# Optimization experiments

Measured on AMD Instinct MI355X. Metric: run time of the kernel, lower is better.

The kernel has to match this reference:

```python
import jax, jax.numpy as jnp
import numpy as np

SEQ_LEN = 12
E, H, BOTTLE = 64, 128, 1024
G, P = 64, 24
B = G * P
EPS = 1e-12  # F.normalize eps


def setup_inputs() -> dict:
    key = jax.random.key(0)
    ks = jax.random.split(key, 24)
    r = lambda k, s: (jax.random.normal(k, s, dtype=jnp.float32) * 0.1)
    starts = np.arange(G, dtype=np.int64) * P
    seq_start_end = jnp.asarray(np.stack([starts, starts + P], axis=1))
    return {
        'last_pos': jax.random.normal(ks[0], (B, 2), dtype=jnp.float32),
        'last_pos_rel': jax.random.normal(ks[1], (B, 2), dtype=jnp.float32),
        'h0': jax.random.normal(ks[2], (1, B, H), dtype=jnp.float32),
        'c0': jax.random.normal(ks[3], (1, B, H), dtype=jnp.float32),
        'seq_start_end': seq_start_end,
        # decoder spatial embedding Linear(2, E)
        'W_emb': r(ks[4], (E, 2)), 'b_emb': r(ks[5], (E,)),
        # LSTM(E -> H), gates ordered i,f,g,o as in torch
        'W_ih': r(ks[6], (4 * H, E)), 'W_hh': r(ks[7], (4 * H, H)),
        'b_ih': r(ks[8], (4 * H,)), 'b_hh': r(ks[9], (4 * H,)),
        # hidden2pos Linear(H, 2)
        'W_pos': r(ks[10], (2, H)), 'b_pos': r(ks[11], (2,)),
        # pool_net spatial embedding Linear(2, E)
        'Wp_emb': r(ks[12], (E, 2)), 'bp_emb': r(ks[13], (E,)),
        # pool_net mlp_pre_pool: (E+H)->512->1024, ReLU
        'Wp1': r(ks[14], (512, E + H)), 'bp1': r(ks[15], (512,)),
        'Wp2': r(ks[16], (BOTTLE, 512)), 'bp2': r(ks[17], (BOTTLE,)),
        # decoder mlp: (H+BOTTLE)->1024->H, ReLU
        'Wm1': r(ks[18], (1024, H + BOTTLE)), 'bm1': r(ks[19], (1024,)),
        'Wm2': r(ks[20], (H, 1024)), 'bm2': r(ks[21], (H,)),
    }


def reference(last_pos, last_pos_rel, h0, c0, seq_start_end,
              W_emb, b_emb, W_ih, W_hh, b_ih, b_hh, W_pos, b_pos,
              Wp_emb, bp_emb, Wp1, bp1, Wp2, bp2, Wm1, bm1, Wm2, bm2):
    batch = last_pos.shape[0]
    n_grp = seq_start_end.shape[0]
    n_ped = batch // n_grp  # equal contiguous groups -> static reshape
    h_dim = h0.shape[-1]

    def pool_net(h, pos):
        # h: [B,H], pos: [B,2]; groups are contiguous slices of size n_ped
        pos_g = pos.reshape(n_grp, n_ped, 2)
        hid_g = h.reshape(n_grp, n_ped, h_dim)
        # rel[g,i,j] = pos[g,j] - pos[g,i]  (torch repeat semantics)
        rel = pos_g[:, None, :, :] - pos_g[:, :, None, :]  # [G,P,P,2]
        nrm = jnp.linalg.norm(rel, axis=-1, keepdims=True)
        rel = rel / jnp.maximum(nrm, EPS)
        emb = rel @ Wp_emb.T + bp_emb                       # [G,P,P,E]
        hid_b = jnp.broadcast_to(hid_g[:, None, :, :], (n_grp, n_ped, n_ped, h_dim))
        x = jnp.concatenate([emb, hid_b], axis=-1)          # [G,P,P,E+H]
        x = jax.nn.relu(x @ Wp1.T + bp1)
        x = jax.nn.relu(x @ Wp2.T + bp2)                    # [G,P,P,1024]
        return jnp.max(x, axis=2).reshape(batch, -1)        # max over j

    def lstm_step(x, h, c):
        gates = x @ W_ih.T + b_ih + h @ W_hh.T + b_hh
        i, f, g, o = jnp.split(gates, 4, axis=-1)
        c = jax.nn.sigmoid(f) * c + jax.nn.sigmoid(i) * jnp.tanh(g)
        h = jax.nn.sigmoid(o) * jnp.tanh(c)
        return h, c

    def step(carry, _):
        h, c, lp, dec_in = carry
        h, c = lstm_step(dec_in, h, c)
        rel_pos = h @ W_pos.T + b_pos          # [B,2]
        curr_pos = rel_pos + lp
        pool_h = pool_net(h, curr_pos)         # [B,1024]
        dh = jnp.concatenate([h, pool_h], axis=1)
        dh = jax.nn.relu(dh @ Wm1.T + bm1)
        h = jax.nn.relu(dh @ Wm2.T + bm2)      # refreshed hidden state
        dec_in = rel_pos @ W_emb.T + b_emb
        return (h, c, curr_pos, dec_in), rel_pos

    dec_in0 = last_pos_rel @ W_emb.T + b_emb
    (h, c, lp, di), rels = jax.lax.scan(
        step, (h0[0], c0[0], last_pos, dec_in0), None, length=SEQ_LEN)
    return rels, h[None]  # ([seq_len,B,2], [1,B,H])
```

## Files before the change

### kernel.cpp

```cpp
#include <hip/hip_runtime.h>
#include <hip/hip_bf16.h>

typedef __attribute__((ext_vector_type(4))) float f32x4;
typedef __attribute__((ext_vector_type(8))) _Float16 f16x8;

static __device__ __forceinline__ unsigned short h2u(_Float16 h) {
  union { _Float16 h; unsigned short u; } v; v.h = h; return v.u;
}


__global__ void cvt_split(const float* __restrict__ src, _Float16* __restrict__ dst, int n) {
  int i = blockIdx.x * 256 + threadIdx.x;
  if (i < n) {
    float x = src[i];
    _Float16 h = (_Float16)x;
    dst[i] = h;
    dst[(size_t)n + i] = (_Float16)(x - (float)h);
  }
}

__global__ void build_wg(const float* __restrict__ W_ih, const float* __restrict__ W_hh,
                         _Float16* __restrict__ Wg) {
  int i = blockIdx.x * 256 + threadIdx.x;
  if (i < 512 * 192) {
    int r = i / 192, k = i % 192;
    float v = (k < 64) ? W_ih[r * 64 + k] : W_hh[r * 128 + (k - 64)];
    _Float16 h = (_Float16)v;
    Wg[i] = h;
    Wg[512 * 192 + i] = (_Float16)(v - (float)h);
  }
}

__global__ void build_wp1b(const float* __restrict__ Wp1, _Float16* __restrict__ W) {
  int i = blockIdx.x * 256 + threadIdx.x;
  if (i < 512 * 128) {
    int r = i >> 7, k = i & 127;
    float v = Wp1[r * 192 + 64 + k];
    _Float16 h = (_Float16)v;
    W[i] = h;
    W[512 * 128 + i] = (_Float16)(v - (float)h);
  }
}

__global__ void build_w2f(const float* __restrict__ Wp2, _Float16* __restrict__ W2f) {
  int idx = blockIdx.x * 256 + threadIdx.x;
  if (idx >= 65536) return;
  int l = idx & 63;
  int c = (idx >> 6) & 15;
  int T = idx >> 10;
  int n = T * 16 + (l & 15);
  int kbase = c * 32 + (l >> 4) * 8;
  size_t dst = ((size_t)((T * 16 + c) * 2) * 64 + l) * 8;
  for (int e = 0; e < 8; e++) {
    float v = Wp2[(size_t)n * 512 + kbase + e];
    _Float16 h = (_Float16)v;
    W2f[dst + e] = h;
    W2f[dst + 512 + e] = (_Float16)(v - (float)h);
  }
}

__global__ void build_misc(const float* __restrict__ Wp1, const float* __restrict__ Wp_emb,
                           const float* __restrict__ bp_emb, const float* __restrict__ bp1,
                           const float* __restrict__ b_ih, const float* __restrict__ b_hh,
                           float* __restrict__ Uc, float* __restrict__ c1,
                           float* __restrict__ bias_g) {
  int r = blockIdx.x * 256 + threadIdx.x;
  if (r < 512) {
    float u0 = 0.f, u1 = 0.f, cc = 0.f;
    for (int e = 0; e < 64; e++) {
      float w = Wp1[r * 192 + e];
      u0 += w * Wp_emb[e * 2 + 0];
      u1 += w * Wp_emb[e * 2 + 1];
      cc += w * bp_emb[e];
    }
    Uc[r * 2 + 0] = u0;
    Uc[r * 2 + 1] = u1;
    c1[r] = bp1[r] + cc;
    bias_g[r] = b_ih[r] + b_hh[r];
  }
}

__global__ void init_state(const float* __restrict__ lp, const float* __restrict__ lpr,
                           const float* __restrict__ h0, const float* __restrict__ c0,
                           const float* __restrict__ W_emb, const float* __restrict__ b_emb,
                           _Float16* __restrict__ A_lstm, size_t PL_AL,
                           float* __restrict__ c_state, float* __restrict__ curr_pos) {
  int row = blockIdx.x;
  int t = threadIdx.x;
  float v;
  if (t < 64) {
    v = lpr[row * 2] * W_emb[t * 2] + lpr[row * 2 + 1] * W_emb[t * 2 + 1] + b_emb[t];
  } else {
    int u = t - 64;
    v = h0[(size_t)row * 128 + u];
    c_state[(size_t)row * 128 + u] = c0[(size_t)row * 128 + u];
  }
  _Float16 h = (_Float16)v;
  A_lstm[(size_t)row * 192 + t] = h;
  A_lstm[PL_AL + (size_t)row * 192 + t] = (_Float16)(v - (float)h);
  if (t < 2) curr_pos[row * 2 + t] = lp[row * 2 + t];
}


__global__ __launch_bounds__(256) void gemm_f16s(
    const _Float16* __restrict__ A, size_t aPl, int lda,
    const _Float16* __restrict__ B, size_t bPl, int ldb,
    const float* __restrict__ bias,
    float* __restrict__ outF, int ldoF,
    _Float16* __restrict__ outS, size_t oPl, int ldoS,
    int K, int relu) {
  __shared__ _Float16 Ah[64][40], Al[64][40], Bh[64][40], Bl[64][40];
  const int tid = threadIdx.x;
  const int lane = tid & 63;
  const int wid = tid >> 6;
  const int wm = wid & 1, wn = wid >> 1;
  const int m0 = blockIdx.x * 64, n0 = blockIdx.y * 64;

  f32x4 acc[2][2];
#pragma unroll
  for (int a = 0; a < 2; a++)
#pragma unroll
    for (int b = 0; b < 2; b++) acc[a][b] = (f32x4){0.f, 0.f, 0.f, 0.f};

  const int srow = tid >> 2, sc = (tid & 3) * 8;
  for (int k0 = 0; k0 < K; k0 += 32) {
    const _Float16* ap = A + (size_t)(m0 + srow) * lda + k0 + sc;
    const _Float16* bp = B + (size_t)(n0 + srow) * ldb + k0 + sc;
    *(uint4*)&Ah[srow][sc] = *(const uint4*)ap;
    *(uint4*)&Al[srow][sc] = *(const uint4*)(ap + aPl);
    *(uint4*)&Bh[srow][sc] = *(const uint4*)bp;
    *(uint4*)&Bl[srow][sc] = *(const uint4*)(bp + bPl);
    __syncthreads();
    const int ar = wm * 32 + (lane & 15), br = wn * 32 + (lane & 15), kk = (lane >> 4) * 8;
    f16x8 ah0 = *(const f16x8*)&Ah[ar][kk];
    f16x8 ah1 = *(const f16x8*)&Ah[ar + 16][kk];
    f16x8 al0 = *(const f16x8*)&Al[ar][kk];
    f16x8 al1 = *(const f16x8*)&Al[ar + 16][kk];
    f16x8 bh0 = *(const f16x8*)&Bh[br][kk];
    f16x8 bh1 = *(const f16x8*)&Bh[br + 16][kk];
    f16x8 bl0 = *(const f16x8*)&Bl[br][kk];
    f16x8 bl1 = *(const f16x8*)&Bl[br + 16][kk];
    acc[0][0] = __builtin_amdgcn_mfma_f32_16x16x32_f16(ah0, bh0, acc[0][0], 0, 0, 0);
    acc[0][0] = __builtin_amdgcn_mfma_f32_16x16x32_f16(ah0, bl0, acc[0][0], 0, 0, 0);
    acc[0][0] = __builtin_amdgcn_mfma_f32_16x16x32_f16(al0, bh0, acc[0][0], 0, 0, 0);
    acc[0][1] = __builtin_amdgcn_mfma_f32_16x16x32_f16(ah0, bh1, acc[0][1], 0, 0, 0);
    acc[0][1] = __builtin_amdgcn_mfma_f32_16x16x32_f16(ah0, bl1, acc[0][1], 0, 0, 0);
    acc[0][1] = __builtin_amdgcn_mfma_f32_16x16x32_f16(al0, bh1, acc[0][1], 0, 0, 0);
    acc[1][0] = __builtin_amdgcn_mfma_f32_16x16x32_f16(ah1, bh0, acc[1][0], 0, 0, 0);
    acc[1][0] = __builtin_amdgcn_mfma_f32_16x16x32_f16(ah1, bl0, acc[1][0], 0, 0, 0);
    acc[1][0] = __builtin_amdgcn_mfma_f32_16x16x32_f16(al1, bh0, acc[1][0], 0, 0, 0);
    acc[1][1] = __builtin_amdgcn_mfma_f32_16x16x32_f16(ah1, bh1, acc[1][1], 0, 0, 0);
    acc[1][1] = __builtin_amdgcn_mfma_f32_16x16x32_f16(ah1, bl1, acc[1][1], 0, 0, 0);
    acc[1][1] = __builtin_amdgcn_mfma_f32_16x16x32_f16(al1, bh1, acc[1][1], 0, 0, 0);
    __syncthreads();
  }
#pragma unroll
  for (int mi = 0; mi < 2; mi++)
#pragma unroll
    for (int ni = 0; ni < 2; ni++)
#pragma unroll
      for (int r = 0; r < 4; r++) {
        int row = m0 + wm * 32 + mi * 16 + (lane >> 4) * 4 + r;
        int col = n0 + wn * 32 + ni * 16 + (lane & 15);
        float v = acc[mi][ni][r];
        if (bias) v += bias[col];
        if (relu) v = fmaxf(v, 0.f);
        if (outF) outF[(size_t)row * ldoF + col] = v;
        if (outS) {
          _Float16 h = (_Float16)v;
          outS[(size_t)row * ldoS + col] = h;
          outS[oPl + (size_t)row * ldoS + col] = (_Float16)(v - (float)h);
        }
      }
}


__global__ __launch_bounds__(256) void lstm_pointwise(
    const float* __restrict__ gates, float* __restrict__ c_state,
    _Float16* __restrict__ A_mlp, size_t PL_AM,
    float* __restrict__ curr_pos,
    float* __restrict__ rels_out,
    _Float16* __restrict__ A_lstm, size_t PL_AL,
    const float* __restrict__ W_pos, const float* __restrict__ b_pos,
    const float* __restrict__ W_emb, const float* __restrict__ b_emb) {
  __shared__ float hbuf[16][128];
  __shared__ float rp[16][2];
  int tid = threadIdx.x;
  int r = tid >> 4, l16 = tid & 15;
  int row = blockIdx.x * 16 + r;
  const float* g = gates + (size_t)row * 512;
#pragma unroll
  for (int s = 0; s < 8; s++) {
    int u = l16 + s * 16;
    float gi = g[u], gf = g[128 + u], gg = g[256 + u], go = g[384 + u];
    float si = 1.f / (1.f + expf(-gi));
    float sf = 1.f / (1.f + expf(-gf));
    float so = 1.f / (1.f + expf(-go));
    float c = sf * c_state[(size_t)row * 128 + u] + si * tanhf(gg);
    c_state[(size_t)row * 128 + u] = c;
    float h = so * tanhf(c);
    hbuf[r][u] = h;
    _Float16 hh = (_Float16)h;
    A_mlp[(size_t)row * 1152 + u] = hh;
    A_mlp[PL_AM + (size_t)row * 1152 + u] = (_Float16)(h - (float)hh);
  }
  __syncthreads();
  if (tid < 32) {
    int rr = tid >> 1, o = tid & 1;
    int rowg = blockIdx.x * 16 + rr;
    float s = b_pos[o];
    const float* w = W_pos + o * 128;
    for (int k = 0; k < 128; k++) s += hbuf[rr][k] * w[k];
    rp[rr][o] = s;
    rels_out[(size_t)rowg * 2 + o] = s;
    curr_pos[(size_t)rowg * 2 + o] += s;
  }
  __syncthreads();
#pragma unroll
  for (int s = 0; s < 4; s++) {
    int u = l16 + s * 16;
    float v = rp[r][0] * W_emb[u * 2] + rp[r][1] * W_emb[u * 2 + 1] + b_emb[u];
    _Float16 hh = (_Float16)v;
    A_lstm[(size_t)row * 192 + u] = hh;
    A_lstm[PL_AL + (size_t)row * 192 + u] = (_Float16)(v - (float)hh);
  }
}


__global__ __launch_bounds__(512) void pool_gemm(
    const float* __restrict__ hpart,
    const float* __restrict__ curr_pos,
    const float* __restrict__ Uc,
    const _Float16* __restrict__ W2f,
    const float* __restrict__ bp2,
    _Float16* __restrict__ A_mlp, size_t oPl) {
  __shared__ _Float16 Ah[96][40], Al[96][40];
  __shared__ float Us0[96], Us1[96];
  __shared__ int pool_tile[4][256];
  int b = blockIdx.x;
  int nt = b & 3;
  int it = (b >> 2) % 6;
  int g = b / 24;
  int tid = threadIdx.x;
  int lane = tid & 63, wid = tid >> 6;
  int wm = wid & 1, wn = wid >> 1;

  int* pt = &pool_tile[0][0];
  pt[tid] = 0;
  pt[tid + 512] = 0;

  if (tid < 96) {
    int r = tid;
    int i = it * 4 + r / 24;
    int j = r % 24;
    float pix = curr_pos[(g * 24 + i) * 2 + 0];
    float piy = curr_pos[(g * 24 + i) * 2 + 1];
    float dx = curr_pos[(g * 24 + j) * 2 + 0] - pix;
    float dy = curr_pos[(g * 24 + j) * 2 + 1] - piy;
    float nrm = sqrtf(dx * dx + dy * dy);
    float inv = 1.f / fmaxf(nrm, 1e-12f);
    Us0[r] = dx * inv;
    Us1[r] = dy * inv;
  }

  f32x4 acc[3][4];
#pragma unroll
  for (int a = 0; a < 3; a++)
#pragma unroll
    for (int c = 0; c < 4; c++) acc[a][c] = (f32x4){0.f, 0.f, 0.f, 0.f};

  const int kc = (2 * tid) & 31;
  const int rb = tid >> 4;

  for (int c16 = 0; c16 < 16; c16++) {
    const int k0 = c16 * 32;
    f16x8 bh[4], bl[4];
#pragma unroll
    for (int ni = 0; ni < 4; ni++) {
      int T = nt * 16 + wn * 4 + ni;
      const _Float16* fb = W2f + ((size_t)(T * 16 + c16) * 2 * 64 + lane) * 8;
      bh[ni] = *(const f16x8*)fb;
      bl[ni] = *(const f16x8*)(fb + 512);
    }
    __syncthreads();
#pragma unroll
    for (int s = 0; s < 3; s++) {
      int r = s * 32 + rb;
      int j = r % 24;
      float2 hp = *(const float2*)(hpart + ((size_t)(g * 24 + j)) * 512 + k0 + kc);
      float4 uc = *(const float4*)(Uc + (size_t)(k0 + kc) * 2);
      float u0 = Us0[r], u1 = Us1[r];
      float v0 = fmaxf(hp.x + u0 * uc.x + u1 * uc.y, 0.f);
      float v1 = fmaxf(hp.y + u0 * uc.z + u1 * uc.w, 0.f);
      _Float16 h0v = (_Float16)v0, h1v = (_Float16)v1;
      _Float16 l0v = (_Float16)(v0 - (float)h0v), l1v = (_Float16)(v1 - (float)h1v);
      *(unsigned int*)&Ah[r][kc] = (unsigned int)h2u(h0v) | ((unsigned int)h2u(h1v) << 16);
      *(unsigned int*)&Al[r][kc] = (unsigned int)h2u(l0v) | ((unsigned int)h2u(l1v) << 16);
    }
    __syncthreads();
    const int kk = (lane >> 4) * 8;
    f16x8 ah[3], al[3];
#pragma unroll
    for (int mi = 0; mi < 3; mi++) {
      int ar = wm * 48 + mi * 16 + (lane & 15);
      ah[mi] = *(const f16x8*)&Ah[ar][kk];
      al[mi] = *(const f16x8*)&Al[ar][kk];
    }
#pragma unroll
    for (int mi = 0; mi < 3; mi++)
#pragma unroll
      for (int ni = 0; ni < 4; ni++) {
        acc[mi][ni] = __builtin_amdgcn_mfma_f32_16x16x32_f16(ah[mi], bh[ni], acc[mi][ni], 0, 0, 0);
        acc[mi][ni] = __builtin_amdgcn_mfma_f32_16x16x32_f16(ah[mi], bl[ni], acc[mi][ni], 0, 0, 0);
        acc[mi][ni] = __builtin_amdgcn_mfma_f32_16x16x32_f16(al[mi], bh[ni], acc[mi][ni], 0, 0, 0);
      }
  }
  __syncthreads();
#pragma unroll
  for (int mi = 0; mi < 3; mi++)
#pragma unroll
    for (int ni = 0; ni < 4; ni++)
#pragma unroll
      for (int r = 0; r < 4; r++) {
        int rl = wm * 48 + mi * 16 + (lane >> 4) * 4 + r;
        int il = rl / 24;
        int nl = wn * 64 + ni * 16 + (lane & 15);
        float z = fmaxf(acc[mi][ni][r] + bp2[nt * 256 + nl], 0.f);
        atomicMax(&pool_tile[il][nl], __float_as_int(z));
      }
  __syncthreads();
  for (int idx = tid; idx < 1024; idx += 512) {
    int il = idx >> 8, nl = idx & 255;
    int row = g * 24 + it * 4 + il;
    float z = __int_as_float(pool_tile[il][nl]);
    _Float16 h = (_Float16)z;
    A_mlp[(size_t)row * 1152 + 128 + nt * 256 + nl] = h;
    A_mlp[oPl + (size_t)row * 1152 + 128 + nt * 256 + nl] = (_Float16)(z - (float)h);
  }
}


extern "C" void kernel_launch(void* const* d_in, const int* in_sizes, int n_in,
                              void* d_out, int out_size, void* d_ws, size_t ws_size,
                              hipStream_t stream) {
  (void)in_sizes; (void)n_in; (void)out_size; (void)ws_size;
  const float* last_pos     = (const float*)d_in[0];
  const float* last_pos_rel = (const float*)d_in[1];
  const float* h0    = (const float*)d_in[2];
  const float* c0    = (const float*)d_in[3];
  const float* W_emb = (const float*)d_in[5];
  const float* b_emb = (const float*)d_in[6];
  const float* W_ih  = (const float*)d_in[7];
  const float* W_hh  = (const float*)d_in[8];
  const float* b_ih  = (const float*)d_in[9];
  const float* b_hh  = (const float*)d_in[10];
  const float* W_pos = (const float*)d_in[11];
  const float* b_pos = (const float*)d_in[12];
  const float* Wp_emb = (const float*)d_in[13];
  const float* bp_emb = (const float*)d_in[14];
  const float* Wp1 = (const float*)d_in[15];
  const float* bp1 = (const float*)d_in[16];
  const float* Wp2 = (const float*)d_in[17];
  const float* bp2 = (const float*)d_in[18];
  const float* Wm1 = (const float*)d_in[19];
  const float* bm1 = (const float*)d_in[20];
  const float* Wm2 = (const float*)d_in[21];
  const float* bm2 = (const float*)d_in[22];

  const size_t PL_WG   = 512 * 192;
  const size_t PL_WP1B = 512 * 128;
  const size_t PL_WM1  = (size_t)1024 * 1152;
  const size_t PL_WM2  = (size_t)128 * 1024;
  const size_t PL_AL   = (size_t)1536 * 192;
  const size_t PL_AM   = (size_t)1536 * 1152;
  const size_t PL_DH   = (size_t)1536 * 1024;

  char* ws = (char*)d_ws;
  size_t off = 0;
  auto alloc = [&](size_t bytes) -> void* {
    void* p = ws + off;
    off = (off + bytes + 255) & ~(size_t)255;
    return p;
  };
  _Float16* Wg_s   = (_Float16*)alloc(PL_WG * 2 * 2);
  _Float16* Wp1b_s = (_Float16*)alloc(PL_WP1B * 2 * 2);
  _Float16* W2f    = (_Float16*)alloc((size_t)1024 * 512 * 2 * 2);
  _Float16* Wm1_s  = (_Float16*)alloc(PL_WM1 * 2 * 2);
  _Float16* Wm2_s  = (_Float16*)alloc(PL_WM2 * 2 * 2);
  float* Uc     = (float*)alloc(512 * 2 * 4);
  float* c1     = (float*)alloc(512 * 4);
  float* bias_g = (float*)alloc(512 * 4);
  _Float16* A_lstm = (_Float16*)alloc(PL_AL * 2 * 2);
  float* gates   = (float*)alloc((size_t)1536 * 512 * 4);
  float* c_state = (float*)alloc((size_t)1536 * 128 * 4);
  _Float16* A_mlp = (_Float16*)alloc(PL_AM * 2 * 2);
  float* curr_pos = (float*)alloc(1536 * 2 * 4);
  float* hpart = (float*)alloc((size_t)1536 * 512 * 4);
  _Float16* dh = (_Float16*)alloc(PL_DH * 2 * 2);

  float* rels = (float*)d_out;
  float* h_out = ((float*)d_out) + 12 * 1536 * 2;

  build_w2f<<<256, 256, 0, stream>>>(Wp2, W2f);
  cvt_split<<<(1179648 + 255) / 256, 256, 0, stream>>>(Wm1, Wm1_s, 1179648);
  cvt_split<<<(131072 + 255) / 256, 256, 0, stream>>>(Wm2, Wm2_s, 131072);
  build_wg<<<(512 * 192 + 255) / 256, 256, 0, stream>>>(W_ih, W_hh, Wg_s);
  build_wp1b<<<(512 * 128 + 255) / 256, 256, 0, stream>>>(Wp1, Wp1b_s);
  build_misc<<<2, 256, 0, stream>>>(Wp1, Wp_emb, bp_emb, bp1, b_ih, b_hh, Uc, c1, bias_g);
  init_state<<<1536, 192, 0, stream>>>(last_pos, last_pos_rel, h0, c0, W_emb, b_emb,
                                       A_lstm, PL_AL, c_state, curr_pos);

  for (int t = 0; t < 12; t++) {
    gemm_f16s<<<dim3(24, 8), 256, 0, stream>>>(A_lstm, PL_AL, 192, Wg_s, PL_WG, 192, bias_g,
                                               gates, 512, (_Float16*)nullptr, 0, 0, 192, 0);
    lstm_pointwise<<<96, 256, 0, stream>>>(gates, c_state, A_mlp, PL_AM, curr_pos,
                                           rels + (size_t)t * 1536 * 2, A_lstm, PL_AL,
                                           W_pos, b_pos, W_emb, b_emb);
    gemm_f16s<<<dim3(24, 8), 256, 0, stream>>>(A_mlp, PL_AM, 1152, Wp1b_s, PL_WP1B, 128, c1,
                                               hpart, 512, (_Float16*)nullptr, 0, 0, 128, 0);
    pool_gemm<<<1536, 512, 0, stream>>>(hpart, curr_pos, Uc, W2f, bp2, A_mlp, PL_AM);
    gemm_f16s<<<dim3(24, 16), 256, 0, stream>>>(A_mlp, PL_AM, 1152, Wm1_s, PL_WM1, 1152, bm1,
                                                (float*)nullptr, 0, dh, PL_DH, 1024, 1152, 1);
    float* houtF = (t == 11) ? h_out : (float*)nullptr;
    gemm_f16s<<<dim3(24, 2), 256, 0, stream>>>(dh, PL_DH, 1024, Wm2_s, PL_WM2, 1024, bm2,
                                               houtF, 128, A_lstm + 64, PL_AL, 192, 1024, 1);
  }
}
```

Measured before the change: 2.129 ms.

## Prefragment GEMM weights into MFMA layout and pipeline pool_gemm A-tile builds

All GEMM weight matrices are now reordered once into an MFMA-fragment layout, so each wave loads its B operands straight from global memory into registers. This removes the B staging through shared memory and halves LDS use in the generic GEMM, which is also templated on K and ReLU. pool_gemm gets a triple-buffered shared A tile, so building the next K-chunk overlaps the current chunk's MFMAs. The cost is more register pressure, redundant global B loads across the M-blocks, and slightly more setup work.

```diff
diff --git a/kernel.cpp b/kernel.cpp
--- a/kernel.cpp
+++ b/kernel.cpp
@@ -8,16 +8,8 @@
   union { _Float16 h; unsigned short u; } v; v.h = h; return v.u;
 }
 
-
-__global__ void cvt_split(const float* __restrict__ src, _Float16* __restrict__ dst, int n) {
-  int i = blockIdx.x * 256 + threadIdx.x;
-  if (i < n) {
-    float x = src[i];
-    _Float16 h = (_Float16)x;
-    dst[i] = h;
-    dst[(size_t)n + i] = (_Float16)(x - (float)h);
-  }
-}
+#define MFMA16(a, b, c) __builtin_amdgcn_mfma_f32_16x16x32_f16(a, b, c, 0, 0, 0)
+
 
 __global__ void build_wg(const float* __restrict__ W_ih, const float* __restrict__ W_hh,
                          _Float16* __restrict__ Wg) {
@@ -42,20 +34,43 @@
   }
 }
 
-__global__ void build_w2f(const float* __restrict__ Wp2, _Float16* __restrict__ W2f) {
+__global__ void refrag_f32(const float* __restrict__ W, _Float16* __restrict__ F,
+                           int N, int Kc) {
   int idx = blockIdx.x * 256 + threadIdx.x;
-  if (idx >= 65536) return;
+  int total = (N >> 4) * Kc * 64;
+  if (idx >= total) return;
   int l = idx & 63;
-  int c = (idx >> 6) & 15;
-  int T = idx >> 10;
+  int c = (idx >> 6) % Kc;
+  int T = (idx >> 6) / Kc;
   int n = T * 16 + (l & 15);
-  int kbase = c * 32 + (l >> 4) * 8;
-  size_t dst = ((size_t)((T * 16 + c) * 2) * 64 + l) * 8;
+  int k = c * 32 + (l >> 4) * 8;
+  int K = Kc * 32;
+  const float* src = W + (size_t)n * K + k;
+  _Float16* dst = F + ((size_t)((T * Kc + c) * 2) * 64 + l) * 8;
   for (int e = 0; e < 8; e++) {
-    float v = Wp2[(size_t)n * 512 + kbase + e];
+    float v = src[e];
     _Float16 h = (_Float16)v;
-    W2f[dst + e] = h;
-    W2f[dst + 512 + e] = (_Float16)(v - (float)h);
+    dst[e] = h;
+    dst[512 + e] = (_Float16)(v - (float)h);
+  }
+}
+
+__global__ void refrag_planes(const _Float16* __restrict__ Ws, size_t plane,
+                              _Float16* __restrict__ F, int N, int Kc) {
+  int idx = blockIdx.x * 256 + threadIdx.x;
+  int total = (N >> 4) * Kc * 64;
+  if (idx >= total) return;
+  int l = idx & 63;
+  int c = (idx >> 6) % Kc;
+  int T = (idx >> 6) / Kc;
+  int n = T * 16 + (l & 15);
+  int k = c * 32 + (l >> 4) * 8;
+  int K = Kc * 32;
+  const _Float16* src = Ws + (size_t)n * K + k;
+  _Float16* dst = F + ((size_t)((T * Kc + c) * 2) * 64 + l) * 8;
+  for (int e = 0; e < 8; e++) {
+    dst[e] = src[e];
+    dst[512 + e] = src[plane + e];
   }
 }
 
@@ -102,14 +117,15 @@
 }
 
 
-__global__ __launch_bounds__(256) void gemm_f16s(
+template <int K, int RELU>
+__global__ __launch_bounds__(256) void gemm_f16f(
     const _Float16* __restrict__ A, size_t aPl, int lda,
-    const _Float16* __restrict__ B, size_t bPl, int ldb,
+    const _Float16* __restrict__ Bf,
     const float* __restrict__ bias,
     float* __restrict__ outF, int ldoF,
-    _Float16* __restrict__ outS, size_t oPl, int ldoS,
-    int K, int relu) {
-  __shared__ _Float16 Ah[64][40], Al[64][40], Bh[64][40], Bl[64][40];
+    _Float16* __restrict__ outS, size_t oPl, int ldoS) {
+  constexpr int Kc = K / 32;
+  __shared__ _Float16 Ah[64][40], Al[64][40];
   const int tid = threadIdx.x;
   const int lane = tid & 63;
   const int wid = tid >> 6;
@@ -123,35 +139,38 @@
     for (int b = 0; b < 2; b++) acc[a][b] = (f32x4){0.f, 0.f, 0.f, 0.f};
 
   const int srow = tid >> 2, sc = (tid & 3) * 8;
-  for (int k0 = 0; k0 < K; k0 += 32) {
+  const int ar = wm * 32 + (lane & 15);
+  const int kk = (lane >> 4) * 8;
+  const int T0 = (n0 >> 4) + wn * 2;
+
+  for (int c = 0; c < Kc; c++) {
+    const int k0 = c * 32;
     const _Float16* ap = A + (size_t)(m0 + srow) * lda + k0 + sc;
-    const _Float16* bp = B + (size_t)(n0 + srow) * ldb + k0 + sc;
-    *(uint4*)&Ah[srow][sc] = *(const uint4*)ap;
-    *(uint4*)&Al[srow][sc] = *(const uint4*)(ap + aPl);
-    *(uint4*)&Bh[srow][sc] = *(const uint4*)bp;
-    *(uint4*)&Bl[srow][sc] = *(const uint4*)(bp + bPl);
+    uint4 avh = *(const uint4*)ap;
+    uint4 avl = *(const uint4*)(ap + aPl);
+    const _Float16* fb0 = Bf + ((size_t)((T0 * Kc + c) * 2) * 64 + lane) * 8;
+    const _Float16* fb1 = Bf + ((size_t)(((T0 + 1) * Kc + c) * 2) * 64 + lane) * 8;
+    f16x8 bh0 = *(const f16x8*)fb0, bl0 = *(const f16x8*)(fb0 + 512);
+    f16x8 bh1 = *(const f16x8*)fb1, bl1 = *(const f16x8*)(fb1 + 512);
+    *(uint4*)&Ah[srow][sc] = avh;
+    *(uint4*)&Al[srow][sc] = avl;
     __syncthreads();
-    const int ar = wm * 32 + (lane & 15), br = wn * 32 + (lane & 15), kk = (lane >> 4) * 8;
     f16x8 ah0 = *(const f16x8*)&Ah[ar][kk];
     f16x8 ah1 = *(const f16x8*)&Ah[ar + 16][kk];
     f16x8 al0 = *(const f16x8*)&Al[ar][kk];
     f16x8 al1 = *(const f16x8*)&Al[ar + 16][kk];
-    f16x8 bh0 = *(const f16x8*)&Bh[br][kk];
-    f16x8 bh1 = *(const f16x8*)&Bh[br + 16][kk];
-    f16x8 bl0 = *(const f16x8*)&Bl[br][kk];
-    f16x8 bl1 = *(const f16x8*)&Bl[br + 16][kk];
-    acc[0][0] = __builtin_amdgcn_mfma_f32_16x16x32_f16(ah0, bh0, acc[0][0], 0, 0, 0);
-    acc[0][0] = __builtin_amdgcn_mfma_f32_16x16x32_f16(ah0, bl0, acc[0][0], 0, 0, 0);
-    acc[0][0] = __builtin_amdgcn_mfma_f32_16x16x32_f16(al0, bh0, acc[0][0], 0, 0, 0);
-    acc[0][1] = __builtin_amdgcn_mfma_f32_16x16x32_f16(ah0, bh1, acc[0][1], 0, 0, 0);
-    acc[0][1] = __builtin_amdgcn_mfma_f32_16x16x32_f16(ah0, bl1, acc[0][1], 0, 0, 0);
-    acc[0][1] = __builtin_amdgcn_mfma_f32_16x16x32_f16(al0, bh1, acc[0][1], 0, 0, 0);
-    acc[1][0] = __builtin_amdgcn_mfma_f32_16x16x32_f16(ah1, bh0, acc[1][0], 0, 0, 0);
-    acc[1][0] = __builtin_amdgcn_mfma_f32_16x16x32_f16(ah1, bl0, acc[1][0], 0, 0, 0);
-    acc[1][0] = __builtin_amdgcn_mfma_f32_16x16x32_f16(al1, bh0, acc[1][0], 0, 0, 0);
-    acc[1][1] = __builtin_amdgcn_mfma_f32_16x16x32_f16(ah1, bh1, acc[1][1], 0, 0, 0);
-    acc[1][1] = __builtin_amdgcn_mfma_f32_16x16x32_f16(ah1, bl1, acc[1][1], 0, 0, 0);
-    acc[1][1] = __builtin_amdgcn_mfma_f32_16x16x32_f16(al1, bh1, acc[1][1], 0, 0, 0);
+    acc[0][0] = MFMA16(ah0, bh0, acc[0][0]);
+    acc[0][0] = MFMA16(ah0, bl0, acc[0][0]);
+    acc[0][0] = MFMA16(al0, bh0, acc[0][0]);
+    acc[0][1] = MFMA16(ah0, bh1, acc[0][1]);
+    acc[0][1] = MFMA16(ah0, bl1, acc[0][1]);
+    acc[0][1] = MFMA16(al0, bh1, acc[0][1]);
+    acc[1][0] = MFMA16(ah1, bh0, acc[1][0]);
+    acc[1][0] = MFMA16(ah1, bl0, acc[1][0]);
+    acc[1][0] = MFMA16(al1, bh0, acc[1][0]);
+    acc[1][1] = MFMA16(ah1, bh1, acc[1][1]);
+    acc[1][1] = MFMA16(ah1, bl1, acc[1][1]);
+    acc[1][1] = MFMA16(al1, bh1, acc[1][1]);
     __syncthreads();
   }
 #pragma unroll
@@ -164,7 +183,7 @@
         int col = n0 + wn * 32 + ni * 16 + (lane & 15);
         float v = acc[mi][ni][r];
         if (bias) v += bias[col];
-        if (relu) v = fmaxf(v, 0.f);
+        if (RELU) v = fmaxf(v, 0.f);
         if (outF) outF[(size_t)row * ldoF + col] = v;
         if (outS) {
           _Float16 h = (_Float16)v;
@@ -234,16 +253,16 @@
     const _Float16* __restrict__ W2f,
     const float* __restrict__ bp2,
     _Float16* __restrict__ A_mlp, size_t oPl) {
-  __shared__ _Float16 Ah[96][40], Al[96][40];
+  __shared__ _Float16 Ah[3][96][40], Al[3][96][40];
   __shared__ float Us0[96], Us1[96];
   __shared__ int pool_tile[4][256];
-  int b = blockIdx.x;
-  int nt = b & 3;
-  int it = (b >> 2) % 6;
-  int g = b / 24;
-  int tid = threadIdx.x;
-  int lane = tid & 63, wid = tid >> 6;
-  int wm = wid & 1, wn = wid >> 1;
+  const int b = blockIdx.x;
+  const int nt = b & 3;
+  const int it = (b >> 2) % 6;
+  const int g = b / 24;
+  const int tid = threadIdx.x;
+  const int lane = tid & 63, wid = tid >> 6;
+  const int wm = wid & 1, wn = wid >> 1;
 
   int* pt = &pool_tile[0][0];
   pt[tid] = 0;
@@ -262,6 +281,7 @@
     Us0[r] = dx * inv;
     Us1[r] = dy * inv;
   }
+  __syncthreads();
 
   f32x4 acc[3][4];
 #pragma unroll
@@ -271,51 +291,61 @@
 
   const int kc = (2 * tid) & 31;
   const int rb = tid >> 4;
-
-  for (int c16 = 0; c16 < 16; c16++) {
+  const int j0 = rb % 24, j1 = (rb + 32) % 24, j2 = (rb + 64) % 24;
+  const float* hp_g = hpart + (size_t)g * 24 * 512;
+
+  auto buildA = [&](int c16, int bi) {
     const int k0 = c16 * 32;
-    f16x8 bh[4], bl[4];
-#pragma unroll
-    for (int ni = 0; ni < 4; ni++) {
-      int T = nt * 16 + wn * 4 + ni;
-      const _Float16* fb = W2f + ((size_t)(T * 16 + c16) * 2 * 64 + lane) * 8;
-      bh[ni] = *(const f16x8*)fb;
-      bl[ni] = *(const f16x8*)(fb + 512);
-    }
-    __syncthreads();
 #pragma unroll
     for (int s = 0; s < 3; s++) {
       int r = s * 32 + rb;
-      int j = r % 24;
-      float2 hp = *(const float2*)(hpart + ((size_t)(g * 24 + j)) * 512 + k0 + kc);
+      int j = (s == 0) ? j0 : (s == 1 ? j1 : j2);
+      float2 hp = *(const float2*)(hp_g + (size_t)j * 512 + k0 + kc);
       float4 uc = *(const float4*)(Uc + (size_t)(k0 + kc) * 2);
       float u0 = Us0[r], u1 = Us1[r];
       float v0 = fmaxf(hp.x + u0 * uc.x + u1 * uc.y, 0.f);
       float v1 = fmaxf(hp.y + u0 * uc.z + u1 * uc.w, 0.f);
       _Float16 h0v = (_Float16)v0, h1v = (_Float16)v1;
       _Float16 l0v = (_Float16)(v0 - (float)h0v), l1v = (_Float16)(v1 - (float)h1v);
-      *(unsigned int*)&Ah[r][kc] = (unsigned int)h2u(h0v) | ((unsigned int)h2u(h1v) << 16);
-      *(unsigned int*)&Al[r][kc] = (unsigned int)h2u(l0v) | ((unsigned int)h2u(l1v) << 16);
+      *(unsigned int*)&Ah[bi][r][kc] = (unsigned int)h2u(h0v) | ((unsigned int)h2u(h1v) << 16);
+      *(unsigned int*)&Al[bi][r][kc] = (unsigned int)h2u(l0v) | ((unsigned int)h2u(l1v) << 16);
     }
+  };
+
+  buildA(0, 0);
+  __syncthreads();
+
+  const int kk = (lane >> 4) * 8;
+  const int Tb = nt * 16 + wn * 4;
+  int bcur = 0;
+  for (int c = 0; c < 16; c++) {
+    f16x8 bh[4], bl[4];
+#pragma unroll
+    for (int ni = 0; ni < 4; ni++) {
+      const _Float16* fb = W2f + ((size_t)(((Tb + ni) * 16 + c) * 2) * 64 + lane) * 8;
+      bh[ni] = *(const f16x8*)fb;
+      bl[ni] = *(const f16x8*)(fb + 512);
+    }
+    int bnext = bcur + 1; if (bnext == 3) bnext = 0;
+    if (c < 15) buildA(c + 1, bnext);
+    f16x8 ah[3], al[3];
+#pragma unroll
+    for (int mi = 0; mi < 3; mi++) {
+      int arr = wm * 48 + mi * 16 + (lane & 15);
+      ah[mi] = *(const f16x8*)&Ah[bcur][arr][kk];
+      al[mi] = *(const f16x8*)&Al[bcur][arr][kk];
+    }
+#pragma unroll
+    for (int mi = 0; mi < 3; mi++)
+#pragma unroll
+      for (int ni = 0; ni < 4; ni++) {
+        acc[mi][ni] = MFMA16(ah[mi], bh[ni], acc[mi][ni]);
+        acc[mi][ni] = MFMA16(ah[mi], bl[ni], acc[mi][ni]);
+        acc[mi][ni] = MFMA16(al[mi], bh[ni], acc[mi][ni]);
+      }
     __syncthreads();
-    const int kk = (lane >> 4) * 8;
-    f16x8 ah[3], al[3];
-#pragma unroll
-    for (int mi = 0; mi < 3; mi++) {
-      int ar = wm * 48 + mi * 16 + (lane & 15);
-      ah[mi] = *(const f16x8*)&Ah[ar][kk];
-      al[mi] = *(const f16x8*)&Al[ar][kk];
-    }
-#pragma unroll
-    for (int mi = 0; mi < 3; mi++)
-#pragma unroll
-      for (int ni = 0; ni < 4; ni++) {
-        acc[mi][ni] = __builtin_amdgcn_mfma_f32_16x16x32_f16(ah[mi], bh[ni], acc[mi][ni], 0, 0, 0);
-        acc[mi][ni] = __builtin_amdgcn_mfma_f32_16x16x32_f16(ah[mi], bl[ni], acc[mi][ni], 0, 0, 0);
-        acc[mi][ni] = __builtin_amdgcn_mfma_f32_16x16x32_f16(al[mi], bh[ni], acc[mi][ni], 0, 0, 0);
-      }
-  }
-  __syncthreads();
+    bcur = bnext;
+  }
 #pragma unroll
   for (int mi = 0; mi < 3; mi++)
 #pragma unroll
@@ -367,13 +397,9 @@
   const float* Wm2 = (const float*)d_in[21];
   const float* bm2 = (const float*)d_in[22];
 
-  const size_t PL_WG   = 512 * 192;
-  const size_t PL_WP1B = 512 * 128;
-  const size_t PL_WM1  = (size_t)1024 * 1152;
-  const size_t PL_WM2  = (size_t)128 * 1024;
-  const size_t PL_AL   = (size_t)1536 * 192;
-  const size_t PL_AM   = (size_t)1536 * 1152;
-  const size_t PL_DH   = (size_t)1536 * 1024;
+  const size_t PL_AL = (size_t)1536 * 192;
+  const size_t PL_AM = (size_t)1536 * 1152;
+  const size_t PL_DH = (size_t)1536 * 1024;
 
   char* ws = (char*)d_ws;
   size_t off = 0;
@@ -382,11 +408,13 @@
     off = (off + bytes + 255) & ~(size_t)255;
     return p;
   };
-  _Float16* Wg_s   = (_Float16*)alloc(PL_WG * 2 * 2);
-  _Float16* Wp1b_s = (_Float16*)alloc(PL_WP1B * 2 * 2);
-  _Float16* W2f    = (_Float16*)alloc((size_t)1024 * 512 * 2 * 2);
-  _Float16* Wm1_s  = (_Float16*)alloc(PL_WM1 * 2 * 2);
-  _Float16* Wm2_s  = (_Float16*)alloc(PL_WM2 * 2 * 2);
+  _Float16* Wg_s   = (_Float16*)alloc((size_t)512 * 192 * 2 * 2);
+  _Float16* Wp1b_s = (_Float16*)alloc((size_t)512 * 128 * 2 * 2);
+  _Float16* Wg_f   = (_Float16*)alloc((size_t)32 * 6 * 1024 * 2);
+  _Float16* Wp1b_f = (_Float16*)alloc((size_t)32 * 4 * 1024 * 2);
+  _Float16* W2f    = (_Float16*)alloc((size_t)64 * 16 * 1024 * 2);
+  _Float16* Wm1_f  = (_Float16*)alloc((size_t)64 * 36 * 1024 * 2);
+  _Float16* Wm2_f  = (_Float16*)alloc((size_t)8 * 32 * 1024 * 2);
   float* Uc     = (float*)alloc(512 * 2 * 4);
   float* c1     = (float*)alloc(512 * 4);
   float* bias_g = (float*)alloc(512 * 4);
@@ -401,28 +429,30 @@
   float* rels = (float*)d_out;
   float* h_out = ((float*)d_out) + 12 * 1536 * 2;
 
-  build_w2f<<<256, 256, 0, stream>>>(Wp2, W2f);
-  cvt_split<<<(1179648 + 255) / 256, 256, 0, stream>>>(Wm1, Wm1_s, 1179648);
-  cvt_split<<<(131072 + 255) / 256, 256, 0, stream>>>(Wm2, Wm2_s, 131072);
-  build_wg<<<(512 * 192 + 255) / 256, 256, 0, stream>>>(W_ih, W_hh, Wg_s);
-  build_wp1b<<<(512 * 128 + 255) / 256, 256, 0, stream>>>(Wp1, Wp1b_s);
+  build_wg<<<(98304 + 255) / 256, 256, 0, stream>>>(W_ih, W_hh, Wg_s);
+  build_wp1b<<<(65536 + 255) / 256, 256, 0, stream>>>(Wp1, Wp1b_s);
+  refrag_planes<<<(12288 + 255) / 256, 256, 0, stream>>>(Wg_s, 98304, Wg_f, 512, 6);
+  refrag_planes<<<(8192 + 255) / 256, 256, 0, stream>>>(Wp1b_s, 65536, Wp1b_f, 512, 4);
+  refrag_f32<<<(65536 + 255) / 256, 256, 0, stream>>>(Wp2, W2f, 1024, 16);
+  refrag_f32<<<(147456 + 255) / 256, 256, 0, stream>>>(Wm1, Wm1_f, 1024, 36);
+  refrag_f32<<<(16384 + 255) / 256, 256, 0, stream>>>(Wm2, Wm2_f, 128, 32);
   build_misc<<<2, 256, 0, stream>>>(Wp1, Wp_emb, bp_emb, bp1, b_ih, b_hh, Uc, c1, bias_g);
   init_state<<<1536, 192, 0, stream>>>(last_pos, last_pos_rel, h0, c0, W_emb, b_emb,
                                        A_lstm, PL_AL, c_state, curr_pos);
 
   for (int t = 0; t < 12; t++) {
-    gemm_f16s<<<dim3(24, 8), 256, 0, stream>>>(A_lstm, PL_AL, 192, Wg_s, PL_WG, 192, bias_g,
-                                               gates, 512, (_Float16*)nullptr, 0, 0, 192, 0);
+    gemm_f16f<192, 0><<<dim3(24, 8), 256, 0, stream>>>(
+        A_lstm, PL_AL, 192, Wg_f, bias_g, gates, 512, (_Float16*)nullptr, 0, 0);
     lstm_pointwise<<<96, 256, 0, stream>>>(gates, c_state, A_mlp, PL_AM, curr_pos,
                                            rels + (size_t)t * 1536 * 2, A_lstm, PL_AL,
                                            W_pos, b_pos, W_emb, b_emb);
-    gemm_f16s<<<dim3(24, 8), 256, 0, stream>>>(A_mlp, PL_AM, 1152, Wp1b_s, PL_WP1B, 128, c1,
-                                               hpart, 512, (_Float16*)nullptr, 0, 0, 128, 0);
+    gemm_f16f<128, 0><<<dim3(24, 8), 256, 0, stream>>>(
+        A_mlp, PL_AM, 1152, Wp1b_f, c1, hpart, 512, (_Float16*)nullptr, 0, 0);
     pool_gemm<<<1536, 512, 0, stream>>>(hpart, curr_pos, Uc, W2f, bp2, A_mlp, PL_AM);
-    gemm_f16s<<<dim3(24, 16), 256, 0, stream>>>(A_mlp, PL_AM, 1152, Wm1_s, PL_WM1, 1152, bm1,
-                                                (float*)nullptr, 0, dh, PL_DH, 1024, 1152, 1);
+    gemm_f16f<1152, 1><<<dim3(24, 16), 256, 0, stream>>>(
+        A_mlp, PL_AM, 1152, Wm1_f, bm1, (float*)nullptr, 0, dh, PL_DH, 1024);
     float* houtF = (t == 11) ? h_out : (float*)nullptr;
-    gemm_f16s<<<dim3(24, 2), 256, 0, stream>>>(dh, PL_DH, 1024, Wm2_s, PL_WM2, 1024, bm2,
-                                               houtF, 128, A_lstm + 64, PL_AL, 192, 1024, 1);
-  }
-}
+    gemm_f16f<1024, 1><<<dim3(24, 2), 256, 0, stream>>>(
+        dh, PL_DH, 1024, Wm2_f, bm2, houtF, 128, A_lstm + 64, PL_AL, 192);
+  }
+}
```

Measured after the change: 2.392 ms. 1.12x slower.
